# Optimization experiments

Measured on AMD Instinct MI355X. Metric: run time of the kernel, lower is better.

The kernel has to match this reference:

```python
import jax, jax.numpy as jnp
import numpy as np

DIM = 128
N = 2048
M = 2048


def setup_inputs() -> dict:
    key = jax.random.key(0)
    k1, k2, k3, k4, k5, k6 = jax.random.split(key, 6)
    s1 = 1.0 / np.sqrt(2 * DIM)  # torch Linear default init bound
    s2 = 1.0 / np.sqrt(DIM)
    return {
        "z_i": jax.random.normal(k1, (N, DIM), dtype=jnp.float32),
        "z_j": jax.random.normal(k2, (M, DIM), dtype=jnp.float32),
        "W1": jax.random.uniform(k3, (2 * DIM, DIM), minval=-s1, maxval=s1, dtype=jnp.float32),
        "b1": jax.random.uniform(k4, (DIM,), minval=-s1, maxval=s1, dtype=jnp.float32),
        "W2": jax.random.uniform(k5, (DIM, 1), minval=-s2, maxval=s2, dtype=jnp.float32),
        "b2": jax.random.uniform(k6, (1,), minval=-s2, maxval=s2, dtype=jnp.float32),
    }


def reference(z_i, z_j, W1, b1, W2, b2):
    # Linear(cat([zi, zj])) == zi @ W1[:dim] + zj @ W1[dim:] + b1 -- same math
    # as the torch module, without materializing the [N, M, 2*dim] concat.
    hi = z_i @ W1[:DIM]  # [N, dim]
    hj = z_j @ W1[DIM:]  # [M, dim]
    h = jax.nn.relu(hi[:, None, :] + hj[None, :, :] + b1)  # [N, M, dim]
    out = h @ W2 + b2  # [N, M, 1]
    return out[..., 0]  # [N, M]
```

## Files before the change

kernel.cpp:

```cpp
#include <hip/hip_runtime.h>

#define DIM 128
#define NROWS 2048
#define NDP 64

typedef float v2f __attribute__((ext_vector_type(2)));
typedef _Float16 h2 __attribute__((ext_vector_type(2)));

static __device__ __forceinline__ h2 u2h(unsigned u) { return __builtin_bit_cast(h2, u); }
static __device__ __forceinline__ unsigned h2u(h2 h) { return __builtin_bit_cast(unsigned, h); }

__global__ __launch_bounds__(256) void prep_kernel(
    const float* __restrict__ z_i, const float* __restrict__ z_j,
    const float* __restrict__ W1, const float* __restrict__ b1,
    unsigned* __restrict__ hi2T, unsigned* __restrict__ hj2T) {
  __shared__ float zs[8 * DIM];

  const int t = threadIdx.x;
  const int side = blockIdx.y;
  const int rowbase = blockIdx.x * 8;

  const float* z = (side ? z_j : z_i) + (size_t)rowbase * DIM;
  ((float4*)zs)[t] = ((const float4*)z)[t];
  __syncthreads();

  const int dp = t & 63;
  const int rg = t >> 6;
  const float* wcol = W1 + side * (DIM * DIM) + dp * 2;
  const float* z0 = zs + (rg * 2) * DIM;
  const float* z1 = z0 + DIM;

  v2f acc0 = {0.f, 0.f}, acc1 = {0.f, 0.f};
#pragma unroll 8
  for (int k = 0; k < DIM; ++k) {
    const v2f wv = *(const v2f*)(wcol + (size_t)k * DIM);
    const float a = z0[k], b = z1[k];
    acc0 = __builtin_elementwise_fma(wv, (v2f){a, a}, acc0);
    acc1 = __builtin_elementwise_fma(wv, (v2f){b, b}, acc1);
  }

  if (side) {
    const v2f bb = *(const v2f*)(b1 + dp * 2);
    acc0 += bb;
    acc1 += bb;
  }
  unsigned* dst = (side ? hj2T : hi2T) + (size_t)dp * NROWS + rowbase + rg * 2;
  dst[0] = h2u((h2){(_Float16)acc0.x, (_Float16)acc0.y});
  dst[1] = h2u((h2){(_Float16)acc1.x, (_Float16)acc1.y});
}

__global__ __launch_bounds__(256, 4) void score_kernel(
    const unsigned* __restrict__ hi2T, const unsigned* __restrict__ hj2T,
    const float* __restrict__ W2, const float* __restrict__ b2p,
    float* __restrict__ out) {
  __shared__ unsigned his2[NDP * 64];
  __shared__ unsigned hjs2[NDP * 64];
  __shared__ unsigned w2s[NDP];

  const int t = threadIdx.x;
  const int ibase = blockIdx.y * 64;
  const int jbase = blockIdx.x * 64;
  const float bias = *b2p;

#pragma unroll
  for (int rep = 0; rep < 4; ++rep) {
    const int idx = rep * 256 + t;
    const int dp = idx >> 4, c = (idx & 15) * 4;
    *(uint4*)(his2 + dp * 64 + c) =
        *(const uint4*)(hi2T + (size_t)dp * NROWS + ibase + c);
    *(uint4*)(hjs2 + dp * 64 + c) =
        *(const uint4*)(hj2T + (size_t)dp * NROWS + jbase + c);
  }
  if (t < NDP) {
    const v2f wp = *(const v2f*)(W2 + t * 2);
    w2s[t] = h2u((h2){(_Float16)wp.x, (_Float16)wp.y});
  }
  __syncthreads();

  const int tx = t & 15;
  const int ty = t >> 4;

  float acc[4][4];
#pragma unroll
  for (int ii = 0; ii < 4; ++ii)
#pragma unroll
    for (int jj = 0; jj < 4; ++jj) acc[ii][jj] = 0.f;

  const h2 zero = {(_Float16)0.f, (_Float16)0.f};
#pragma unroll 2
  for (int dpg = 0; dpg < 16; ++dpg) {
    const uint4 w4 = *(const uint4*)(w2s + dpg * 4);
    const h2 wp[4] = {u2h(w4.x), u2h(w4.y), u2h(w4.z), u2h(w4.w)};
#pragma unroll
    for (int q = 0; q < 4; ++q) {
      const int dp = dpg * 4 + q;
      const uint4 hu = *(const uint4*)(his2 + dp * 64 + ty * 4);
      const uint4 ju = *(const uint4*)(hjs2 + dp * 64 + tx * 4);
      const h2 hiv[4] = {u2h(hu.x), u2h(hu.y), u2h(hu.z), u2h(hu.w)};
      const h2 hjv[4] = {u2h(ju.x), u2h(ju.y), u2h(ju.z), u2h(ju.w)};
#pragma unroll
      for (int ii = 0; ii < 4; ++ii) {
#pragma unroll
        for (int jj = 0; jj < 4; ++jj) {
          h2 s = hiv[ii] + hjv[jj];
          s = __builtin_elementwise_max(s, zero);
          acc[ii][jj] = __builtin_amdgcn_fdot2(s, wp[q], acc[ii][jj], false);
        }
      }
    }
  }

#pragma unroll
  for (int ii = 0; ii < 4; ++ii) {
    const int i = ibase + ty * 4 + ii;
    float* o = out + (size_t)i * NROWS + jbase + tx * 4;
    const float4 ov = {acc[ii][0] + bias, acc[ii][1] + bias,
                       acc[ii][2] + bias, acc[ii][3] + bias};
    *(float4*)o = ov;
  }
}

extern "C" void kernel_launch(void* const* d_in, const int* in_sizes, int n_in,
                              void* d_out, int out_size, void* d_ws, size_t ws_size,
                              hipStream_t stream) {
  const float* z_i = (const float*)d_in[0];
  const float* z_j = (const float*)d_in[1];
  const float* W1  = (const float*)d_in[2];
  const float* b1  = (const float*)d_in[3];
  const float* W2  = (const float*)d_in[4];
  const float* b2  = (const float*)d_in[5];
  float* out = (float*)d_out;

  unsigned* hi2T = (unsigned*)d_ws;
  unsigned* hj2T = hi2T + (size_t)NDP * NROWS;

  prep_kernel<<<dim3(256, 2), 256, 0, stream>>>(z_i, z_j, W1, b1, hi2T, hj2T);
  score_kernel<<<dim3(32, 32), 256, 0, stream>>>(hi2T, hj2T, W2, b2, out);
}
```

Measured before the change: 105.3 us.

## Fuse projection GEMM into score kernel using MFMA per-tile recomputation

Removes the separate prep kernel and workspace round trip. Each score block now computes its own 64-row slices of z_i@W1 and z_j@W1 with fp16 MFMA 16x16x32 instructions, staging W1 transposed into LDS as fp16. This trades a second launch and global writes and reads for redundant per-block recomputation of the projections and repeated W1 loads. Higher LDS usage lowers the occupancy bound from 4 to 3 blocks.

```diff
diff --git a/kernel.cpp b/kernel.cpp
--- a/kernel.cpp
+++ b/kernel.cpp
@@ -3,56 +3,21 @@
 #define DIM 128
 #define NROWS 2048
 #define NDP 64
+#define WSTRIDE 72
 
-typedef float v2f __attribute__((ext_vector_type(2)));
 typedef _Float16 h2 __attribute__((ext_vector_type(2)));
+typedef _Float16 f16x8 __attribute__((ext_vector_type(8)));
+typedef float f32x4 __attribute__((ext_vector_type(4)));
 
 static __device__ __forceinline__ h2 u2h(unsigned u) { return __builtin_bit_cast(h2, u); }
 static __device__ __forceinline__ unsigned h2u(h2 h) { return __builtin_bit_cast(unsigned, h); }
 
-__global__ __launch_bounds__(256) void prep_kernel(
+__global__ __launch_bounds__(256, 3) void fused_kernel(
     const float* __restrict__ z_i, const float* __restrict__ z_j,
     const float* __restrict__ W1, const float* __restrict__ b1,
-    unsigned* __restrict__ hi2T, unsigned* __restrict__ hj2T) {
-  __shared__ float zs[8 * DIM];
-
-  const int t = threadIdx.x;
-  const int side = blockIdx.y;
-  const int rowbase = blockIdx.x * 8;
-
-  const float* z = (side ? z_j : z_i) + (size_t)rowbase * DIM;
-  ((float4*)zs)[t] = ((const float4*)z)[t];
-  __syncthreads();
-
-  const int dp = t & 63;
-  const int rg = t >> 6;
-  const float* wcol = W1 + side * (DIM * DIM) + dp * 2;
-  const float* z0 = zs + (rg * 2) * DIM;
-  const float* z1 = z0 + DIM;
-
-  v2f acc0 = {0.f, 0.f}, acc1 = {0.f, 0.f};
-#pragma unroll 8
-  for (int k = 0; k < DIM; ++k) {
-    const v2f wv = *(const v2f*)(wcol + (size_t)k * DIM);
-    const float a = z0[k], b = z1[k];
-    acc0 = __builtin_elementwise_fma(wv, (v2f){a, a}, acc0);
-    acc1 = __builtin_elementwise_fma(wv, (v2f){b, b}, acc1);
-  }
-
-  if (side) {
-    const v2f bb = *(const v2f*)(b1 + dp * 2);
-    acc0 += bb;
-    acc1 += bb;
-  }
-  unsigned* dst = (side ? hj2T : hi2T) + (size_t)dp * NROWS + rowbase + rg * 2;
-  dst[0] = h2u((h2){(_Float16)acc0.x, (_Float16)acc0.y});
-  dst[1] = h2u((h2){(_Float16)acc1.x, (_Float16)acc1.y});
-}
-
-__global__ __launch_bounds__(256, 4) void score_kernel(
-    const unsigned* __restrict__ hi2T, const unsigned* __restrict__ hj2T,
     const float* __restrict__ W2, const float* __restrict__ b2p,
     float* __restrict__ out) {
+  __shared__ _Float16 wbuf[DIM * WSTRIDE];
   __shared__ unsigned his2[NDP * 64];
   __shared__ unsigned hjs2[NDP * 64];
   __shared__ unsigned w2s[NDP];
@@ -60,31 +25,95 @@
   const int t = threadIdx.x;
   const int ibase = blockIdx.y * 64;
   const int jbase = blockIdx.x * 64;
-  const float bias = *b2p;
+
+  if (t < NDP)
+    w2s[t] = h2u((h2){(_Float16)W2[2 * t], (_Float16)W2[2 * t + 1]});
+
+  const int w = t >> 6;
+  const int quad = (t >> 4) & 3;
+  const int n = t & 15;
+  const int sd = t & 127;
+  const int sgb = (t >> 7) * 4;
 
 #pragma unroll
-  for (int rep = 0; rep < 4; ++rep) {
-    const int idx = rep * 256 + t;
-    const int dp = idx >> 4, c = (idx & 15) * 4;
-    *(uint4*)(his2 + dp * 64 + c) =
-        *(const uint4*)(hi2T + (size_t)dp * NROWS + ibase + c);
-    *(uint4*)(hjs2 + dp * 64 + c) =
-        *(const uint4*)(hj2T + (size_t)dp * NROWS + jbase + c);
-  }
-  if (t < NDP) {
-    const v2f wp = *(const v2f*)(W2 + t * 2);
-    w2s[t] = h2u((h2){(_Float16)wp.x, (_Float16)wp.y});
+  for (int side = 0; side < 2; ++side) {
+    const float* z = side ? z_j : z_i;
+    const int rbase = side ? jbase : ibase;
+    f32x4 acc[2][4];
+#pragma unroll
+    for (int a = 0; a < 2; ++a)
+#pragma unroll
+      for (int b = 0; b < 4; ++b) acc[a][b] = (f32x4){0.f, 0.f, 0.f, 0.f};
+
+#pragma unroll
+    for (int chunk = 0; chunk < 2; ++chunk) {
+      const int c0 = chunk * 64;
+      __syncthreads();
+#pragma unroll
+      for (int g = 0; g < 4; ++g) {
+        const int gg = sgb + g;
+        const float* wp = W1 + (size_t)(side * DIM + c0 + gg * 8) * DIM + sd;
+        _Float16 v[8];
+#pragma unroll
+        for (int jx = 0; jx < 8; ++jx) v[jx] = (_Float16)wp[jx * DIM];
+        *(f16x8*)(wbuf + sd * WSTRIDE + gg * 8) =
+            (f16x8){v[0], v[1], v[2], v[3], v[4], v[5], v[6], v[7]};
+      }
+      __syncthreads();
+
+#pragma unroll
+      for (int s = 0; s < 2; ++s) {
+        const int kabs = c0 + s * 32;
+        f16x8 af[2];
+#pragma unroll
+        for (int dtl = 0; dtl < 2; ++dtl) {
+          const int d = (2 * w + dtl) * 16 + n;
+          af[dtl] = *(const f16x8*)(wbuf + d * WSTRIDE + (s * 32 + quad * 8));
+        }
+#pragma unroll
+        for (int it = 0; it < 4; ++it) {
+          const float* zp =
+              z + (size_t)(rbase + it * 16 + n) * DIM + kabs + quad * 8;
+          const float4 a = *(const float4*)zp;
+          const float4 b = *(const float4*)(zp + 4);
+          const f16x8 bf = {(_Float16)a.x, (_Float16)a.y, (_Float16)a.z,
+                            (_Float16)a.w, (_Float16)b.x, (_Float16)b.y,
+                            (_Float16)b.z, (_Float16)b.w};
+#pragma unroll
+          for (int dtl = 0; dtl < 2; ++dtl)
+            acc[dtl][it] = __builtin_amdgcn_mfma_f32_16x16x32_f16(
+                af[dtl], bf, acc[dtl][it], 0, 0, 0);
+        }
+      }
+    }
+
+    unsigned* dest = side ? hjs2 : his2;
+#pragma unroll
+    for (int dtl = 0; dtl < 2; ++dtl) {
+      const int dt = 2 * w + dtl;
+      float4 bb = {0.f, 0.f, 0.f, 0.f};
+      if (side) bb = *(const float4*)(b1 + dt * 16 + quad * 4);
+      const int dp0 = dt * 8 + quad * 2;
+#pragma unroll
+      for (int it = 0; it < 4; ++it) {
+        const f32x4 c = acc[dtl][it];
+        const int i = it * 16 + n;
+        dest[dp0 * 64 + i] =
+            h2u((h2){(_Float16)(c.x + bb.x), (_Float16)(c.y + bb.y)});
+        dest[(dp0 + 1) * 64 + i] =
+            h2u((h2){(_Float16)(c.z + bb.z), (_Float16)(c.w + bb.w)});
+      }
+    }
   }
   __syncthreads();
 
   const int tx = t & 15;
   const int ty = t >> 4;
-
-  float acc[4][4];
+  float facc[4][4];
 #pragma unroll
   for (int ii = 0; ii < 4; ++ii)
 #pragma unroll
-    for (int jj = 0; jj < 4; ++jj) acc[ii][jj] = 0.f;
+    for (int jj = 0; jj < 4; ++jj) facc[ii][jj] = 0.f;
 
   const h2 zero = {(_Float16)0.f, (_Float16)0.f};
 #pragma unroll 2
@@ -102,21 +131,20 @@
       for (int ii = 0; ii < 4; ++ii) {
 #pragma unroll
         for (int jj = 0; jj < 4; ++jj) {
-          h2 s = hiv[ii] + hjv[jj];
-          s = __builtin_elementwise_max(s, zero);
-          acc[ii][jj] = __builtin_amdgcn_fdot2(s, wp[q], acc[ii][jj], false);
+          h2 s2 = hiv[ii] + hjv[jj];
+          s2 = __builtin_elementwise_max(s2, zero);
+          facc[ii][jj] = __builtin_amdgcn_fdot2(s2, wp[q], facc[ii][jj], false);
         }
       }
     }
   }
 
+  const float bias = *b2p;
 #pragma unroll
   for (int ii = 0; ii < 4; ++ii) {
-    const int i = ibase + ty * 4 + ii;
-    float* o = out + (size_t)i * NROWS + jbase + tx * 4;
-    const float4 ov = {acc[ii][0] + bias, acc[ii][1] + bias,
-                       acc[ii][2] + bias, acc[ii][3] + bias};
-    *(float4*)o = ov;
+    float* o = out + (size_t)(ibase + ty * 4 + ii) * NROWS + jbase + tx * 4;
+    *(float4*)o = (float4){facc[ii][0] + bias, facc[ii][1] + bias,
+                           facc[ii][2] + bias, facc[ii][3] + bias};
   }
 }
 
@@ -131,9 +159,5 @@
   const float* b2  = (const float*)d_in[5];
   float* out = (float*)d_out;
 
-  unsigned* hi2T = (unsigned*)d_ws;
-  unsigned* hj2T = hi2T + (size_t)NDP * NROWS;
-
-  prep_kernel<<<dim3(256, 2), 256, 0, stream>>>(z_i, z_j, W1, b1, hi2T, hj2T);
-  score_kernel<<<dim3(32, 32), 256, 0, stream>>>(hi2T, hj2T, W2, b2, out);
+  fused_kernel<<<dim3(32, 32), 256, 0, stream>>>(z_i, z_j, W1, b1, W2, b2, out);
 }
```

Result: slower. 120.1 us (+14.0%).
